# Kernel tuning notes

Hardware: AMD Instinct MI355X
Metric: run time of the kernel (lower is better)

The kernel has to match this reference:

```python
import jax, jax.numpy as jnp
import numpy as np

VOC, EMB, C, H, W, ANS = 10000, 300, 24, 8, 8, 1000
HID = 500          # lstm_hidden_size
GH = 100           # g_mlp hidden
B, L = 64, 32
O = H * W          # obj_num
CONCAT = 2 * C + HID  # 548


def setup_inputs() -> dict:
    key = jax.random.key(0)
    ks = jax.random.split(key, 20)
    inp = {}
    inp["sent_batch"] = jax.random.randint(ks[0], (B, L), 0, VOC)
    inp["conv_map_batch"] = jax.random.normal(ks[1], (B, C, H, W), jnp.float32)
    inp["sents_lengths"] = jax.random.randint(ks[2], (B,), 1, L + 1)
    # embedding table with padding_idx=0 zeroed
    emb = jax.random.normal(ks[3], (VOC, EMB), jnp.float32) * 0.02
    inp["embed_table"] = emb.at[0].set(0.0)
    # forward-direction LSTM params (torch gate order i,f,g,o)
    s_ih = 1.0 / np.sqrt(HID)
    inp["W_ih"] = jax.random.uniform(ks[4], (4 * HID, EMB), jnp.float32, -s_ih, s_ih)
    inp["W_hh"] = jax.random.uniform(ks[5], (4 * HID, HID), jnp.float32, -s_ih, s_ih)
    inp["b_ih"] = jax.random.uniform(ks[6], (4 * HID,), jnp.float32, -s_ih, s_ih)
    inp["b_hh"] = jax.random.uniform(ks[7], (4 * HID,), jnp.float32, -s_ih, s_ih)
    # random (non-learned) LSTM initial state, as torch.rand in init_hidden
    inp["h0"] = jax.random.uniform(ks[8], (B, HID), jnp.float32)
    inp["c0"] = jax.random.uniform(ks[9], (B, HID), jnp.float32)
    def lin(k, o, i):
        s = 1.0 / np.sqrt(i)
        kw, kb = jax.random.split(k)
        return (jax.random.uniform(kw, (o, i), jnp.float32, -s, s),
                jax.random.uniform(kb, (o,), jnp.float32, -s, s))
    inp["g1_w"], inp["g1_b"] = lin(ks[10], GH, CONCAT)
    inp["g2_w"], inp["g2_b"] = lin(ks[11], GH, GH)
    inp["f1_w"], inp["f1_b"] = lin(ks[12], GH, GH)
    inp["f2_w"], inp["f2_b"] = lin(ks[13], ANS, GH)
    return inp


def _lstm_final_h(emb, lengths, W_ih, W_hh, b_ih, b_hh, h0, c0):
    # emb: (B, L, EMB); returns final forward hidden at t = length-1 per example
    xs = jnp.swapaxes(emb, 0, 1)  # (L, B, EMB)
    ts = jnp.arange(emb.shape[1])
    bias = b_ih + b_hh
    def step(carry, inp):
        h, c = carry
        xt, t = inp
        gates = xt @ W_ih.T + h @ W_hh.T + bias
        i, f, g, o = jnp.split(gates, 4, axis=-1)
        i, f, o = jax.nn.sigmoid(i), jax.nn.sigmoid(f), jax.nn.sigmoid(o)
        g = jnp.tanh(g)
        c_new = f * c + i * g
        h_new = o * jnp.tanh(c_new)
        m = (t < lengths)[:, None]
        return (jnp.where(m, h_new, h), jnp.where(m, c_new, c)), None
    (h_T, _), _ = jax.lax.scan(step, (h0, c0), (xs, ts))
    return h_T  # (B, HID)


def reference(sent_batch, conv_map_batch, sents_lengths, embed_table,
              W_ih, W_hh, b_ih, b_hh, h0, c0,
              g1_w, g1_b, g2_w, g2_b, f1_w, f1_b, f2_w, f2_b):
    emb = embed_table[sent_batch]  # (B, L, EMB)
    q = _lstm_final_h(emb, sents_lengths, W_ih, W_hh, b_ih, b_hh, h0, c0)  # (B, HID)
    obj = jnp.transpose(conv_map_batch, (0, 2, 3, 1)).reshape(B, O, C)  # (B, O, C)
    # g_mlp layer 1, split to avoid materializing (B, O^2, 548):
    # pair (i,j): cat(q, obj_j, obj_i) -> partial sums broadcast-added
    q_part = q @ g1_w[:, :HID].T                    # (B, GH)
    j_part = obj @ g1_w[:, HID:HID + C].T           # (B, O, GH) -- conv_expand_1 block
    i_part = obj @ g1_w[:, HID + C:].T              # (B, O, GH) -- conv_expand_2 block
    h1 = jax.nn.relu(q_part[:, None, None, :] + i_part[:, :, None, :]
                     + j_part[:, None, :, :] + g1_b)  # (B, O, O, GH)
    h2 = jax.nn.relu(h1 @ g2_w.T + g2_b)              # (B, O, O, GH)
    g_sum = h2.sum(axis=(1, 2))                       # (B, GH)
    f = jax.nn.relu(g_sum @ f1_w.T + f1_b)
    f = jax.nn.relu(f @ f2_w.T + f2_b)                # (B, ANS)
    return jax.nn.log_softmax(f, axis=-1)
```

## Files before the change

### kernel.cpp

```cpp
#include <hip/hip_runtime.h>
#include <cmath>

#define BATCH 64
#define SEQL  32
#define EMBD  300
#define HIDD  500
#define NOBJ  64
#define GHID  100
#define ANSN  1000
#define MCOL  2048

#define GRP    4
#define GBATCH 16
#define BPG    25
#define UPB8   20
#define NBLK   (GRP*BPG)
#define NXG    256
#define SLOTP  32

#define KPADX  328
#define TCH    4

typedef _Float16 half8 __attribute__((ext_vector_type(8)));
typedef float    f32x4 __attribute__((ext_vector_type(4)));

__device__ __forceinline__ float sigmf(float x){ return 1.f/(1.f+expf(-x)); }

__device__ __forceinline__ unsigned long long ld_cc8(const unsigned long long* p){
    return __hip_atomic_load(p, __ATOMIC_RELAXED, __HIP_MEMORY_SCOPE_AGENT);
}
__device__ __forceinline__ void st_cc8(_Float16* p, unsigned long long v){
    __hip_atomic_store((unsigned long long*)p, v, __ATOMIC_RELAXED, __HIP_MEMORY_SCOPE_AGENT);
}
__device__ __forceinline__ float ld_cc4(const float* p){
    return __hip_atomic_load(p, __ATOMIC_RELAXED, __HIP_MEMORY_SCOPE_AGENT);
}
__device__ __forceinline__ void st_cc4(float* p, float v){
    __hip_atomic_store(p, v, __ATOMIC_RELAXED, __HIP_MEMORY_SCOPE_AGENT);
}

__device__ __forceinline__ void gbarA(int* slots, int grp, int ub, int seq)
{
    __syncthreads();
    if (threadIdx.x == 0)
        __hip_atomic_store(slots + (grp*BPG + ub)*SLOTP, seq,
                           __ATOMIC_RELAXED, __HIP_MEMORY_SCOPE_AGENT);
    if (threadIdx.x < BPG){
        int* s = slots + (grp*BPG + threadIdx.x)*SLOTP;
        while (__hip_atomic_load(s, __ATOMIC_RELAXED, __HIP_MEMORY_SCOPE_AGENT) < seq)
            __builtin_amdgcn_s_sleep(1);
    }
    asm volatile("" ::: "memory");
    __syncthreads();
}

__device__ __forceinline__ void pack_store_h(
    _Float16* hF, int buf, int grp, int u0, int w, int lane, float hval)
{
    union { _Float16 f; unsigned short s; } cv;
    cv.f = (_Float16)hval;
    unsigned int h2 = cv.s;
    int base = lane & 15;
    unsigned int x0 = (unsigned int)__shfl((int)h2, base +  0, 64);
    unsigned int x1 = (unsigned int)__shfl((int)h2, base + 16, 64);
    unsigned int x2 = (unsigned int)__shfl((int)h2, base + 32, 64);
    unsigned int x3 = (unsigned int)__shfl((int)h2, base + 48, 64);
    if (lane < 16){
        unsigned long long v = (unsigned long long)(x0 & 0xFFFFu)
                             | ((unsigned long long)(x1 & 0xFFFFu) << 16)
                             | ((unsigned long long)(x2 & 0xFFFFu) << 32)
                             | ((unsigned long long)(x3 & 0xFFFFu) << 48);
        st_cc8(hF + ((size_t)(buf*GRP + grp)*GBATCH + lane)*512 + u0 + w*4, v);
    }
}

__global__ __launch_bounds__(320, 1) void k_mega(
    const int* __restrict__ sent, const float* __restrict__ table,
    const float* __restrict__ Wih, const float* __restrict__ b_ih, const float* __restrict__ b_hh,
    _Float16* __restrict__ hF, float* __restrict__ hqB, float* __restrict__ xgT,
    const float* __restrict__ Whh, const float* __restrict__ h0, const float* __restrict__ c0,
    const int* __restrict__ lens, int* __restrict__ slots, int* __restrict__ xgdone)
{
    __shared__ __align__(16) char smem[102400];

    int tid = threadIdx.x, bid = blockIdx.x;
    int w = tid >> 6, lane = tid & 63;

    if (bid >= NBLK){
        _Float16* Sh  = (_Float16*)smem;
        int*      sidx= (int*)(smem + 41984);
        int xb = bid - NBLK;
        int tc = xb >> 5;
        int n0 = (xb & 31) * 64;
        int rA = lane & 15, kb = lane >> 4;

        for (int i = tid; i < TCH*64; i += 320){
            int tt = i >> 6, b = i & 63;
            sidx[tt*64 + b] = sent[b*SEQL + tc*TCH + tt];
        }
        for (int i = tid; i < 64*75; i += 320){
            int n = i / 75, c4 = i - (i/75)*75;
            float4 v = {0.f,0.f,0.f,0.f};
            if (n0 + n < 2000)
                v = *(const float4*)(Wih + (size_t)(n0+n)*300 + c4*4);
            _Float16* dst = &Sh[n*KPADX + c4*4];
            dst[0]=(_Float16)v.x; dst[1]=(_Float16)v.y; dst[2]=(_Float16)v.z; dst[3]=(_Float16)v.w;
        }
        for (int i = tid; i < 64*20; i += 320){
            int n = i / 20, k = 300 + (i - (i/20)*20);
            Sh[n*KPADX + k] = (_Float16)0.f;
        }
        __syncthreads();
        half8 areg[10];
        float biasr[4];
        if (w < 4){
            #pragma unroll
            for (int ks = 0; ks < 10; ++ks)
                areg[ks] = *(const half8*)&Sh[(w*16 + rA)*KPADX + ks*32 + kb*8];
            #pragma unroll
            for (int r = 0; r < 4; ++r){
                int n = n0 + w*16 + kb*4 + r;
                biasr[r] = (n < 2000) ? b_ih[n] + b_hh[n] : 0.f;
            }
        }
        __syncthreads();

        for (int tt = 0; tt < TCH; ++tt){
            for (int i = tid; i < 64*75; i += 320){
                int m = i / 75, c4 = i - (i/75)*75;
                float4 v = *(const float4*)(table + (size_t)sidx[tt*64 + m]*300 + c4*4);
                _Float16* dst = &Sh[m*KPADX + c4*4];
                dst[0]=(_Float16)v.x; dst[1]=(_Float16)v.y; dst[2]=(_Float16)v.z; dst[3]=(_Float16)v.w;
            }
            for (int i = tid; i < 64*20; i += 320){
                int m = i / 20, k = 300 + (i - (i/20)*20);
                Sh[m*KPADX + k] = (_Float16)0.f;
            }
            __syncthreads();

            if (w < 4){
                f32x4 acc[4] = {};
                #pragma unroll
                for (int ks = 0; ks < 10; ++ks){
                    #pragma unroll
                    for (int mc = 0; mc < 4; ++mc){
                        half8 bf = *(const half8*)&Sh[(mc*16 + rA)*KPADX + ks*32 + kb*8];
                        acc[mc] = __builtin_amdgcn_mfma_f32_16x16x32_f16(areg[ks], bf, acc[mc], 0, 0, 0);
                    }
                }
                #pragma unroll
                for (int r = 0; r < 4; ++r){
                    int n = n0 + w*16 + kb*4 + r;
                    if (n < 2000){
                        #pragma unroll
                        for (int mc = 0; mc < 4; ++mc)
                            st_cc4(xgT + (size_t)n*MCOL + (tc*TCH+tt)*64 + mc*16 + rA,
                                   acc[mc][r] + biasr[r]);
                    }
                }
            }
            __syncthreads();
        }
        if (tid == 0)
            __hip_atomic_fetch_add(xgdone + tc*SLOTP, 1,
                                   __ATOMIC_RELAXED, __HIP_MEMORY_SCOPE_AGENT);
        return;
    }

    _Float16* Wl  = (_Float16*)smem;
    float*    gl  = (float*)(smem + 81920);

    int grp = bid / BPG, ub = bid - grp*BPG;
    int u0  = ub * UPB8;

    int pb  = tid & 15, puu = tid >> 4;
    int pu  = u0 + puu;
    int gb  = grp*GBATCH + pb;
    float cprev = c0[gb*HIDD + pu];
    float hprev = h0[gb*HIDD + pu];
    int   mylen = lens[gb];

    for (int i = tid; i < 80*512; i += 320){
        int m = i >> 9, k = i & 511;
        int g = m / UPB8, uu = m - g*UPB8;
        float v = (k < HIDD) ? Whh[(size_t)(g*HIDD + u0 + uu)*HIDD + k] : 0.f;
        int off = (i*2) ^ ((m & 7) << 4);
        *(_Float16*)((char*)Wl + off) = (_Float16)v;
    }
    pack_store_h(hF, 1, grp, u0, w, lane, hprev);
    if (ub == 0 && tid >= 128 && tid < 224){
        int j = tid - 128;
        int buf = j / 48, r = j - buf*48;
        int b = r / 3, q = r - (r/3)*3;
        st_cc8(hF + ((size_t)(buf*GRP + grp)*GBATCH + b)*512 + 500 + q*4, 0ULL);
    }
    gbarA(slots, grp, ub, 1);

    const int mA = lane & 15, kb = lane >> 4;

    for (int t = 0; t < SEQL; ++t){
        if ((t & 3) == 0){
            if (tid == 0){
                const int* f = xgdone + (t >> 2)*SLOTP;
                while (__hip_atomic_load(f, __ATOMIC_RELAXED, __HIP_MEMORY_SCOPE_AGENT) < 32)
                    __builtin_amdgcn_s_sleep(1);
            }
            asm volatile("" ::: "memory");
            __syncthreads();
        }

        const _Float16* hsrc = hF + (size_t)(((t&1)^1)*GRP + grp)*GBATCH*512;

        float xgv[4];
        #pragma unroll
        for (int g = 0; g < 4; ++g)
            xgv[g] = ld_cc4(xgT + (size_t)(g*HIDD + pu)*MCOL + t*64 + gb);

        if (w < 4){
            half8 bf[4];
            #pragma unroll
            for (int ks4 = 0; ks4 < 4; ++ks4){
                int ke = (w*4 + ks4)*32 + kb*8;
                const unsigned long long* p =
                    (const unsigned long long*)(hsrc + mA*512 + ke);
                union { unsigned long long q[2]; half8 h; } u;
                u.q[0] = ld_cc8(p);
                u.q[1] = ld_cc8(p + 1);
                bf[ks4] = u.h;
            }
            f32x4 acc[5] = {};
            #pragma unroll
            for (int rt = 0; rt < 5; ++rt){
                #pragma unroll
                for (int ks4 = 0; ks4 < 4; ++ks4){
                    int kByte = (w*4 + ks4)*64 + kb*16;
                    int m = rt*16 + mA;
                    int aOff = (m*1024 + kByte) ^ ((m & 7) << 4);
                    half8 af = *(const half8*)((const char*)Wl + aOff);
                    acc[rt] = __builtin_amdgcn_mfma_f32_16x16x32_f16(af, bf[ks4], acc[rt], 0, 0, 0);
                }
            }
            #pragma unroll
            for (int rt = 0; rt < 5; ++rt)
                #pragma unroll
                for (int r = 0; r < 4; ++r)
                    gl[(w*80 + rt*16 + kb*4 + r)*16 + mA] = acc[rt][r];
        }
        __syncthreads();

        {
            float g4[4];
            #pragma unroll
            for (int g = 0; g < 4; ++g){
                int row = g*UPB8 + puu;
                float s = gl[(0*80 + row)*16 + pb] + gl[(1*80 + row)*16 + pb]
                        + gl[(2*80 + row)*16 + pb] + gl[(3*80 + row)*16 + pb];
                s += xgv[g];
                g4[g] = s;
            }
            float si = sigmf(g4[0]), sf = sigmf(g4[1]);
            float tg = tanhf(g4[2]), so = sigmf(g4[3]);
            float cn = sf*cprev + si*tg;
            float hn = so*tanhf(cn);
            if (t < mylen){ cprev = cn; hprev = hn; }
        }
        if (t == SEQL-1){
            hqB[(size_t)gb*512 + pu] = hprev;
        } else {
            pack_store_h(hF, t & 1, grp, u0, w, lane, hprev);
            gbarA(slots, grp, ub, t + 2);
        }
    }
}

__global__ __launch_bounds__(256, 1) void k_pair3(
    const float* __restrict__ hqB, const float* __restrict__ conv,
    const float* __restrict__ g1w, const float* __restrict__ g1b,
    const float* __restrict__ g2w, const float* __restrict__ g2b,
    const float* __restrict__ f1w, const float* __restrict__ f1b,
    const float* __restrict__ f2w, const float* __restrict__ f2b,
    float* __restrict__ part, int* __restrict__ pcnt, float* __restrict__ out)
{
    __shared__ float    convl[24][64];
    __shared__ float    g1ij[100][48];
    __shared__ float    hb[512];
    __shared__ float    qpl[112];
    __shared__ float    jpl[NOBJ][132];
    __shared__ float    basel[16][132];
    __shared__ _Float16 g2h[112][136];
    __shared__ float    redx[4][112];
    __shared__ float    gs[112], fh[112];
    __shared__ float    lg[ANSN];
    __shared__ float    red[4], red2[4];
    __shared__ int      lastf;

    int b  = blockIdx.x >> 2;
    int ic = blockIdx.x & 3;
    int tid = threadIdx.x;
    int w = tid >> 6, lane = tid & 63;
    int ncol = lane & 15, kb = lane >> 4;

    for (int i = tid; i < 24*64; i += 256)
        convl[i>>6][i&63] = conv[((size_t)b*24 + (i>>6))*64 + (i&63)];
    for (int i = tid; i < 100*48; i += 256){
        int n = i/48, c = i - (i/48)*48;
        g1ij[n][c] = g1w[(size_t)n*548 + 500 + c];
    }
    for (int i = tid; i < 512; i += 256) hb[i] = hqB[(size_t)b*512 + i];
    for (int i = tid; i < 112*136; i += 256){
        int n = i/136, k = i - (i/136)*136;
        g2h[n][k] = (n < 100 && k < 100) ? (_Float16)g2w[n*GHID + k] : (_Float16)0.f;
    }
    __syncthreads();

    if (tid < 100){
        const float4* wr = (const float4*)(g1w + (size_t)tid*548);
        float s = g1b[tid];
        #pragma unroll 5
        for (int k4 = 0; k4 < 125; ++k4){
            float4 v = wr[k4];
            s += v.x*hb[k4*4] + v.y*hb[k4*4+1] + v.z*hb[k4*4+2] + v.w*hb[k4*4+3];
        }
        qpl[tid] = s;
    }
    for (int i = tid; i < NOBJ*100; i += 256){
        int o = i / 100, n = i - (i/100)*100;
        float sj = 0.f;
        #pragma unroll
        for (int c = 0; c < 24; ++c) sj += convl[c][o] * g1ij[n][c];
        jpl[o][n] = sj;
    }
    for (int i = tid; i < NOBJ*32; i += 256) jpl[i>>5][100 + (i&31)] = 0.f;
    __syncthreads();

    for (int i = tid; i < 16*132; i += 256){
        int il = i / 132, k = i - (i/132)*132;
        float v = 0.f;
        if (k < 100){
            float si = 0.f;
            int o = ic*16 + il;
            #pragma unroll
            for (int c = 0; c < 24; ++c) si += convl[c][o] * g1ij[k][24+c];
            v = qpl[k] + si;
        }
        basel[il][k] = v;
    }
    float gb7[7];
    #pragma unroll
    for (int nt = 0; nt < 7; ++nt){
        int n = nt*16 + ncol;
        gb7[nt] = (n < 100) ? g2b[n] : 0.f;
    }
    __syncthreads();

    f32x4 sacc[7] = {};
    #pragma unroll
    for (int it = 0; it < 4; ++it){
        int il = w*4 + it;
        #pragma unroll
        for (int jc = 0; jc < 4; ++jc){
            f32x4 acc[7] = {};
            int jrow = jc*16 + ncol;
            #pragma unroll
            for (int ks = 0; ks < 4; ++ks){
                int k0 = ks*32 + kb*8;
                const float* jpp = &jpl[jrow][k0];
                const float* bpp = &basel[il][k0];
                half8 af;
                #pragma unroll
                for (int e = 0; e < 8; ++e)
                    af[e] = (_Float16)fmaxf(jpp[e] + bpp[e], 0.f);
                #pragma unroll
                for (int nt = 0; nt < 7; ++nt){
                    half8 bf = *(const half8*)&g2h[nt*16 + ncol][k0];
                    acc[nt] = __builtin_amdgcn_mfma_f32_16x16x32_f16(af, bf, acc[nt], 0, 0, 0);
                }
            }
            #pragma unroll
            for (int nt = 0; nt < 7; ++nt)
                #pragma unroll
                for (int r = 0; r < 4; ++r)
                    sacc[nt][r] += fmaxf(acc[nt][r] + gb7[nt], 0.f);
        }
    }
    #pragma unroll
    for (int nt = 0; nt < 7; ++nt){
        float s = sacc[nt][0] + sacc[nt][1] + sacc[nt][2] + sacc[nt][3];
        s += __shfl_xor(s, 16);
        s += __shfl_xor(s, 32);
        if (lane < 16) redx[w][nt*16 + lane] = s;
    }
    __syncthreads();
    if (tid < 100){
        float p = redx[0][tid] + redx[1][tid] + redx[2][tid] + redx[3][tid];
        st_cc4(part + (size_t)(b*4 + ic)*GHID + tid, p);
    }
    __syncthreads();

    if (tid == 0){
        int old = __hip_atomic_fetch_add(pcnt + b*SLOTP, 1,
                                         __ATOMIC_ACQ_REL, __HIP_MEMORY_SCOPE_AGENT);
        lastf = (old == 3);
    }
    __syncthreads();
    if (!lastf) return;

    if (tid < 100){
        float s = 0.f;
        #pragma unroll
        for (int ic2 = 0; ic2 < 4; ++ic2)
            s += ld_cc4(part + (size_t)(b*4 + ic2)*GHID + tid);
        gs[tid] = s;
    }
    __syncthreads();
    if (tid < 100){
        const float4* wr = (const float4*)(f1w + (size_t)tid*GHID);
        float s = f1b[tid];
        #pragma unroll 5
        for (int k4 = 0; k4 < 25; ++k4){
            float4 v = wr[k4];
            s += v.x*gs[k4*4] + v.y*gs[k4*4+1] + v.z*gs[k4*4+2] + v.w*gs[k4*4+3];
        }
        fh[tid] = fmaxf(s, 0.f);
    }
    __syncthreads();
    for (int n = tid; n < ANSN; n += 256){
        const float4* wr = (const float4*)(f2w + (size_t)n*GHID);
        float s = f2b[n];
        #pragma unroll 5
        for (int k4 = 0; k4 < 25; ++k4){
            float4 v = wr[k4];
            s += v.x*fh[k4*4] + v.y*fh[k4*4+1] + v.z*fh[k4*4+2] + v.w*fh[k4*4+3];
        }
        lg[n] = fmaxf(s, 0.f);
    }
    __syncthreads();
    float mx = -1e30f;
    for (int n = tid; n < ANSN; n += 256) mx = fmaxf(mx, lg[n]);
    #pragma unroll
    for (int off = 32; off > 0; off >>= 1) mx = fmaxf(mx, __shfl_xor(mx, off));
    if ((tid & 63) == 0) red[tid >> 6] = mx;
    __syncthreads();
    mx = fmaxf(fmaxf(red[0], red[1]), fmaxf(red[2], red[3]));
    float se = 0.f;
    for (int n = tid; n < ANSN; n += 256) se += expf(lg[n]-mx);
    #pragma unroll
    for (int off = 32; off > 0; off >>= 1) se += __shfl_xor(se, off);
    if ((tid & 63) == 0) red2[tid >> 6] = se;
    __syncthreads();
    se = red2[0]+red2[1]+red2[2]+red2[3];
    float lse = logf(se);
    for (int n = tid; n < ANSN; n += 256) out[(size_t)b*ANSN + n] = lg[n] - mx - lse;
}

extern "C" void kernel_launch(void* const* d_in, const int* in_sizes, int n_in,
                              void* d_out, int out_size, void* d_ws, size_t ws_size,
                              hipStream_t stream)
{
    const int*   sent  = (const int*)  d_in[0];
    const float* conv  = (const float*)d_in[1];
    const int*   lens  = (const int*)  d_in[2];
    const float* table = (const float*)d_in[3];
    const float* W_ih  = (const float*)d_in[4];
    const float* W_hh  = (const float*)d_in[5];
    const float* b_ih  = (const float*)d_in[6];
    const float* b_hh  = (const float*)d_in[7];
    const float* h0    = (const float*)d_in[8];
    const float* c0    = (const float*)d_in[9];
    const float* g1_w  = (const float*)d_in[10];
    const float* g1_b  = (const float*)d_in[11];
    const float* g2_w  = (const float*)d_in[12];
    const float* g2_b  = (const float*)d_in[13];
    const float* f1_w  = (const float*)d_in[14];
    const float* f1_b  = (const float*)d_in[15];
    const float* f2_w  = (const float*)d_in[16];
    const float* f2_b  = (const float*)d_in[17];
    float* out = (float*)d_out;

    float* ws    = (float*)d_ws;
    int*   slots = (int*)d_ws;
    int*   xgdone= (int*)d_ws + NBLK*SLOTP;
    int*   pcnt  = (int*)d_ws + NBLK*SLOTP + 8*SLOTP;
    _Float16* hF = (_Float16*)(ws + 16384);
    float* hqB  = ws + 16384 + 32768;
    float* xgT  = hqB + 64*512;
    float* part = xgT + (size_t)4*HIDD*MCOL;

    hipMemsetAsync(slots, 0, (NBLK + 8 + BATCH)*SLOTP*sizeof(int), stream);

    k_mega<<<NBLK + NXG, 320, 0, stream>>>(sent, table, W_ih, b_ih, b_hh,
                                           hF, hqB, xgT, W_hh, h0, c0, lens,
                                           slots, xgdone);

    k_pair3<<<BATCH*4, 256, 0, stream>>>(hqB, conv, g1_w, g1_b, g2_w, g2_b,
                                         f1_w, f1_b, f2_w, f2_b, part, pcnt, out);
}
```

Before: 223.9 us.

## Overlay shared memory, store pair operands in fp16 for two blocks per CU

```diff
diff --git a/kernel.cpp b/kernel.cpp
--- a/kernel.cpp
+++ b/kernel.cpp
@@ -20,6 +20,22 @@
 
 #define KPADX  328
 #define TCH    4
+
+#define SM_CONV   0
+#define SM_G1IJ   6144
+#define SM_HB     25344
+#define SM_QPL    27392
+#define SM_REDX   0
+#define SM_GS     1792
+#define SM_FH     2240
+#define SM_LG     2688
+#define SM_RED    6688
+#define SM_RED2   6704
+#define SM_LASTF  6720
+#define SM_JPL    27840
+#define SM_BASEL  45248
+#define SM_G2H    49600
+#define SM_TOTAL  80064
 
 typedef _Float16 half8 __attribute__((ext_vector_type(8)));
 typedef float    f32x4 __attribute__((ext_vector_type(4)));
@@ -273,7 +289,7 @@
     }
 }
 
-__global__ __launch_bounds__(256, 1) void k_pair3(
+__global__ __launch_bounds__(256, 2) void k_pair4(
     const float* __restrict__ hqB, const float* __restrict__ conv,
     const float* __restrict__ g1w, const float* __restrict__ g1b,
     const float* __restrict__ g2w, const float* __restrict__ g2b,
@@ -281,18 +297,14 @@
     const float* __restrict__ f2w, const float* __restrict__ f2b,
     float* __restrict__ part, int* __restrict__ pcnt, float* __restrict__ out)
 {
-    __shared__ float    convl[24][64];
-    __shared__ float    g1ij[100][48];
-    __shared__ float    hb[512];
-    __shared__ float    qpl[112];
-    __shared__ float    jpl[NOBJ][132];
-    __shared__ float    basel[16][132];
-    __shared__ _Float16 g2h[112][136];
-    __shared__ float    redx[4][112];
-    __shared__ float    gs[112], fh[112];
-    __shared__ float    lg[ANSN];
-    __shared__ float    red[4], red2[4];
-    __shared__ int      lastf;
+    __shared__ __align__(16) char smem[SM_TOTAL];
+    float*    convl = (float*)(smem + SM_CONV);
+    float*    g1ij  = (float*)(smem + SM_G1IJ);
+    float*    hb    = (float*)(smem + SM_HB);
+    float*    qpl   = (float*)(smem + SM_QPL);
+    _Float16* jpl   = (_Float16*)(smem + SM_JPL);
+    _Float16* basel = (_Float16*)(smem + SM_BASEL);
+    _Float16* g2h   = (_Float16*)(smem + SM_G2H);
 
     int b  = blockIdx.x >> 2;
     int ic = blockIdx.x & 3;
@@ -301,15 +313,15 @@
     int ncol = lane & 15, kb = lane >> 4;
 
     for (int i = tid; i < 24*64; i += 256)
-        convl[i>>6][i&63] = conv[((size_t)b*24 + (i>>6))*64 + (i&63)];
+        convl[i] = conv[(size_t)b*24*64 + i];
     for (int i = tid; i < 100*48; i += 256){
-        int n = i/48, c = i - (i/48)*48;
-        g1ij[n][c] = g1w[(size_t)n*548 + 500 + c];
+        int n = i/48, c = i - n*48;
+        g1ij[n*48 + c] = g1w[(size_t)n*548 + 500 + c];
     }
     for (int i = tid; i < 512; i += 256) hb[i] = hqB[(size_t)b*512 + i];
     for (int i = tid; i < 112*136; i += 256){
-        int n = i/136, k = i - (i/136)*136;
-        g2h[n][k] = (n < 100 && k < 100) ? (_Float16)g2w[n*GHID + k] : (_Float16)0.f;
+        int n = i/136, k = i - n*136;
+        g2h[n*136 + k] = (n < 100 && k < 100) ? (_Float16)g2w[n*GHID + k] : (_Float16)0.f;
     }
     __syncthreads();
 
@@ -327,23 +339,24 @@
         int o = i / 100, n = i - (i/100)*100;
         float sj = 0.f;
         #pragma unroll
-        for (int c = 0; c < 24; ++c) sj += convl[c][o] * g1ij[n][c];
-        jpl[o][n] = sj;
-    }
-    for (int i = tid; i < NOBJ*32; i += 256) jpl[i>>5][100 + (i&31)] = 0.f;
-    __syncthreads();
-
-    for (int i = tid; i < 16*132; i += 256){
-        int il = i / 132, k = i - (i/132)*132;
+        for (int c = 0; c < 24; ++c) sj += convl[c*64 + o] * g1ij[n*48 + c];
+        jpl[o*136 + n] = (_Float16)sj;
+    }
+    for (int i = tid; i < NOBJ*36; i += 256)
+        jpl[(i/36)*136 + 100 + (i - (i/36)*36)] = (_Float16)0.f;
+    __syncthreads();
+
+    for (int i = tid; i < 16*136; i += 256){
+        int il = i / 136, k = i - il*136;
         float v = 0.f;
         if (k < 100){
             float si = 0.f;
             int o = ic*16 + il;
             #pragma unroll
-            for (int c = 0; c < 24; ++c) si += convl[c][o] * g1ij[k][24+c];
+            for (int c = 0; c < 24; ++c) si += convl[c*64 + o] * g1ij[k*48 + 24 + c];
             v = qpl[k] + si;
         }
-        basel[il][k] = v;
+        basel[il*136 + k] = (_Float16)v;
     }
     float gb7[7];
     #pragma unroll
@@ -354,25 +367,27 @@
     __syncthreads();
 
     f32x4 sacc[7] = {};
-    #pragma unroll
+    #pragma unroll 1
     for (int it = 0; it < 4; ++it){
         int il = w*4 + it;
-        #pragma unroll
+        #pragma unroll 1
         for (int jc = 0; jc < 4; ++jc){
             f32x4 acc[7] = {};
             int jrow = jc*16 + ncol;
             #pragma unroll
             for (int ks = 0; ks < 4; ++ks){
                 int k0 = ks*32 + kb*8;
-                const float* jpp = &jpl[jrow][k0];
-                const float* bpp = &basel[il][k0];
+                half8 jv = *(const half8*)&jpl[jrow*136 + k0];
+                half8 bv = *(const half8*)&basel[il*136 + k0];
                 half8 af;
                 #pragma unroll
-                for (int e = 0; e < 8; ++e)
-                    af[e] = (_Float16)fmaxf(jpp[e] + bpp[e], 0.f);
+                for (int e = 0; e < 8; ++e){
+                    _Float16 s = jv[e] + bv[e];
+                    af[e] = (s > (_Float16)0.f) ? s : (_Float16)0.f;
+                }
                 #pragma unroll
                 for (int nt = 0; nt < 7; ++nt){
-                    half8 bf = *(const half8*)&g2h[nt*16 + ncol][k0];
+                    half8 bf = *(const half8*)&g2h[(nt*16 + ncol)*136 + k0];
                     acc[nt] = __builtin_amdgcn_mfma_f32_16x16x32_f16(af, bf, acc[nt], 0, 0, 0);
                 }
             }
@@ -383,27 +398,35 @@
                     sacc[nt][r] += fmaxf(acc[nt][r] + gb7[nt], 0.f);
         }
     }
+    float* redx = (float*)(smem + SM_REDX);
     #pragma unroll
     for (int nt = 0; nt < 7; ++nt){
         float s = sacc[nt][0] + sacc[nt][1] + sacc[nt][2] + sacc[nt][3];
         s += __shfl_xor(s, 16);
         s += __shfl_xor(s, 32);
-        if (lane < 16) redx[w][nt*16 + lane] = s;
+        if (lane < 16) redx[w*112 + nt*16 + lane] = s;
     }
     __syncthreads();
     if (tid < 100){
-        float p = redx[0][tid] + redx[1][tid] + redx[2][tid] + redx[3][tid];
+        float p = redx[0*112+tid] + redx[1*112+tid] + redx[2*112+tid] + redx[3*112+tid];
         st_cc4(part + (size_t)(b*4 + ic)*GHID + tid, p);
     }
     __syncthreads();
 
+    int* lastf = (int*)(smem + SM_LASTF);
     if (tid == 0){
         int old = __hip_atomic_fetch_add(pcnt + b*SLOTP, 1,
                                          __ATOMIC_ACQ_REL, __HIP_MEMORY_SCOPE_AGENT);
-        lastf = (old == 3);
-    }
-    __syncthreads();
-    if (!lastf) return;
+        *lastf = (old == 3);
+    }
+    __syncthreads();
+    if (!*lastf) return;
+
+    float* gs  = (float*)(smem + SM_GS);
+    float* fh  = (float*)(smem + SM_FH);
+    float* lg  = (float*)(smem + SM_LG);
+    float* red = (float*)(smem + SM_RED);
+    float* red2= (float*)(smem + SM_RED2);
 
     if (tid < 100){
         float s = 0.f;
@@ -492,6 +515,6 @@
                                            hF, hqB, xgT, W_hh, h0, c0, lens,
                                            slots, xgdone);
 
-    k_pair3<<<BATCH*4, 256, 0, stream>>>(hqB, conv, g1_w, g1_b, g2_w, g2_b,
+    k_pair4<<<BATCH*4, 256, 0, stream>>>(hqB, conv, g1_w, g1_b, g2_w, g2_b,
                                          f1_w, f1_b, f2_w, f2_b, part, pcnt, out);
 }
```

New measurement: 215.0 us. 4.0% less time.
